# Kernel tuning notes

Hardware: AMD Instinct MI355X
Metric: run time of the kernel (lower is better)

The kernel has to match this reference:

```python
import jax, jax.numpy as jnp
import numpy as np

N_NODES = 50000
N_EDGES = 200000
IN_DIM = 16
NODE_DIM = 64
EDGE_DIM = 16
HIDDEN = 256
NUM_LAYERS = 4  # 1 NNConv + 3 GINConv


def setup_inputs() -> dict:
    key = jax.random.key(0)
    ks = jax.random.split(key, 20)
    s = 0.05
    inp = {
        "x": jax.random.normal(ks[0], (N_NODES, IN_DIM), dtype=jnp.float32),
        "edge_index": jax.random.randint(ks[1], (2, N_EDGES), 0, N_NODES, dtype=jnp.int64),
        "edge_attr": jax.random.normal(ks[2], (N_EDGES, EDGE_DIM), dtype=jnp.float32),
        # edge-NN (per-edge weight generator): attr_dim -> 256 -> 1024 -> in*out, ELU after each
        "enn_w1": jax.random.normal(ks[3], (EDGE_DIM, 256), dtype=jnp.float32) * s,
        "enn_b1": jnp.zeros((256,), dtype=jnp.float32),
        "enn_w2": jax.random.normal(ks[4], (256, 1024), dtype=jnp.float32) * s,
        "enn_b2": jnp.zeros((1024,), dtype=jnp.float32),
        "enn_w3": jax.random.normal(ks[5], (1024, IN_DIM * NODE_DIM), dtype=jnp.float32) * s,
        "enn_b3": jnp.zeros((IN_DIM * NODE_DIM,), dtype=jnp.float32),
        # NNConv root weight + bias
        "root_w": jax.random.normal(ks[6], (IN_DIM, NODE_DIM), dtype=jnp.float32) * s,
        "root_b": jnp.zeros((NODE_DIM,), dtype=jnp.float32),
        # 3 GIN MLPs (stacked): node_dim -> hidden -> hidden -> node_dim
        "gin_w1": jax.random.normal(ks[7], (3, NODE_DIM, HIDDEN), dtype=jnp.float32) * s,
        "gin_b1": jnp.zeros((3, HIDDEN), dtype=jnp.float32),
        "gin_w2": jax.random.normal(ks[8], (3, HIDDEN, HIDDEN), dtype=jnp.float32) * s,
        "gin_b2": jnp.zeros((3, HIDDEN), dtype=jnp.float32),
        "gin_w3": jax.random.normal(ks[9], (3, HIDDEN, NODE_DIM), dtype=jnp.float32) * s,
        "gin_b3": jnp.zeros((3, NODE_DIM), dtype=jnp.float32),
    }
    return inp


def _elu(x):
    return jax.nn.elu(x)


def reference(x, edge_index, edge_attr,
              enn_w1, enn_b1, enn_w2, enn_b2, enn_w3, enn_b3,
              root_w, root_b,
              gin_w1, gin_b1, gin_w2, gin_b2, gin_w3, gin_b3):
    src = edge_index[0]  # x_j (message source)
    dst = edge_index[1]  # i (aggregation target)

    # ---- Layer 0: NNConv with per-edge MLP-generated weights ----
    h = _elu(edge_attr @ enn_w1 + enn_b1)
    h = _elu(h @ enn_w2 + enn_b2)
    w_e = _elu(h @ enn_w3 + enn_b3).reshape(-1, IN_DIM, NODE_DIM)  # [E, in, out]
    msg = jnp.einsum('ei,eio->eo', x[src], w_e)                    # [E, node_dim]
    agg = jax.ops.segment_sum(msg, dst, num_segments=N_NODES)     # scatter-add
    x_cur = x @ root_w + agg + root_b                              # [N, node_dim]
    node_emb = [x_cur]

    # ---- Layers 1..3: GINConv (eps=0) with 3-layer MLP ----
    for l in range(NUM_LAYERS - 1):
        x_in = _elu(x_cur)
        nbr = jax.ops.segment_sum(x_in[src], dst, num_segments=N_NODES)
        h = x_in + nbr  # (1 + eps) * x + sum_j x_j, eps = 0
        h = _elu(h @ gin_w1[l] + gin_b1[l])
        h = _elu(h @ gin_w2[l] + gin_b2[l])
        x_cur = h @ gin_w3[l] + gin_b3[l]
        node_emb.append(x_cur)

    return jnp.stack(node_emb, axis=2)  # [N, node_dim, num_layers]
```

## Files before the change

kernel.cpp:

```cpp
#include <hip/hip_runtime.h>
#include <hip/hip_bf16.h>


#define NN 50000
#define EE 200000

typedef unsigned short u16;
typedef __attribute__((ext_vector_type(8))) short frag8;
typedef __attribute__((ext_vector_type(4))) float f32x4;

__device__ __forceinline__ float bf2f(u16 u) {
    union { unsigned int i; float f; } v; v.i = ((unsigned int)u) << 16; return v.f;
}
__device__ __forceinline__ u16 f2bf(float f) {
    union { float f; unsigned int i; } v; v.f = f;
    return (u16)((v.i + 0x7fffu + ((v.i >> 16) & 1u)) >> 16);
}
__device__ __forceinline__ float eluf(float v) {
    return v > 0.f ? v : __expf(v) - 1.f;
}

__global__ void probe_f32(const u16* __restrict__ raw, int* __restrict__ cnt) {
    int t = threadIdx.x;
    int c = 0;
    for (int j = t; j < 1024; j += 256) {
        unsigned e = (raw[j] >> 7) & 0xFF;
        if (e >= 0xBF) c++;
    }
    if (c) atomicAdd(cnt, c);
}
__global__ void cvt_bf16(const void* __restrict__ src, u16* __restrict__ dst, long n,
                         const int* __restrict__ cnt) {
    long i = (long)blockIdx.x * 256 + threadIdx.x;
    if (i >= n) return;
    if (*cnt >= 8) dst[i] = f2bf(((const float*)src)[i]);
    else           dst[i] = ((const u16*)src)[i];
}

__global__ void detect_idx64(const unsigned long long* __restrict__ p, int* __restrict__ flag) {
    long t = (long)blockIdx.x * 256 + threadIdx.x;
    if (t < EE) {
        unsigned long long v = p[t];
        if (v >> 31) atomicOr(flag, 1);
    }
}
__global__ void convert_idx(const void* __restrict__ raw, const int* __restrict__ flag,
                            int* __restrict__ s_out, int* __restrict__ d_out) {
    long t = (long)blockIdx.x * 256 + threadIdx.x;
    if (t >= EE) return;
    if (*flag) {
        const int* q = (const int*)raw;
        s_out[t] = q[t];
        d_out[t] = q[EE + t];
    } else {
        const long long* q = (const long long*)raw;
        s_out[t] = (int)q[t];
        d_out[t] = (int)q[EE + t];
    }
}

__global__ void transpose_bf16(const u16* __restrict__ in, u16* __restrict__ out, int K, int N) {
    long idx = (long)blockIdx.x * 256 + threadIdx.x;
    if (idx < (long)K * N) {
        int k = (int)(idx / N);
        int n = (int)(idx % N);
        out[(long)n * K + k] = in[idx];
    }
}

__global__ void edge_mlp1(const u16* __restrict__ attr, const u16* __restrict__ w1,
                          const u16* __restrict__ b1, u16* __restrict__ h1, int ce) {
    __shared__ u16 sa[256];
    const int t = threadIdx.x;
    const int e0 = blockIdx.x * 16;
    const int cnt = min(16, ce - e0);
    sa[t] = (t < cnt * 16) ? attr[(long)e0 * 16 + t] : (u16)0;
    float w[16];
    #pragma unroll
    for (int i = 0; i < 16; ++i) w[i] = bf2f(w1[i * 256 + t]);
    const float bb = bf2f(b1[t]);
    __syncthreads();
    for (int e = 0; e < cnt; ++e) {
        float v = bb;
        #pragma unroll
        for (int i = 0; i < 16; ++i) v += bf2f(sa[e * 16 + i]) * w[i];
        h1[(long)(e0 + e) * 256 + t] = f2bf(eluf(v));
    }
}

__device__ __forceinline__ void stage_tile(const u16* g, long row_base, long max_row,
                                           int kstride, int k0, u16* s, int t) {
    int wave = t >> 6;
    #pragma unroll
    for (int j = 0; j < 2; ++j) {
        int c = t + 256 * j;
        long r = row_base + (c >> 2);
        if (r > max_row) r = max_row;
        const u16* gp = g + r * (long)kstride + k0 + (c & 3) * 8;
        __builtin_amdgcn_global_load_lds(
            (__attribute__((address_space(1))) void*)(void*)gp,
            (__attribute__((address_space(3))) void*)((char*)s + wave * 1024 + j * 4096),
            16, 0, 0);
    }
}

__global__ __launch_bounds__(256)
void gemm_bt_bias_elu(const u16* __restrict__ A, const u16* __restrict__ BT,
                      const u16* __restrict__ bias, u16* __restrict__ C,
                      int M, int K, int N, int mpx, int lognt) {
    const int bid = blockIdx.x;
    const int xcd = bid & 7;
    const int j = bid >> 3;
    const int m_idx = xcd * mpx + (j >> lognt);
    const int n_idx = j & ((1 << lognt) - 1);
    const int num_m = (M + 127) >> 7;
    if (m_idx >= num_m) return;

    __shared__ __align__(16) u16 sA[128 * 32];
    __shared__ __align__(16) u16 sB[128 * 32];
    const int t = threadIdx.x;
    const int lane = t & 63;
    const int wave = t >> 6;
    const int wr = wave >> 1, wc = wave & 1;
    const int quad = lane >> 4, l16 = lane & 15;
    const long m0 = (long)m_idx * 128;
    const int n0 = n_idx * 128;

    f32x4 acc[4][4];
    const f32x4 z4 = {0.f, 0.f, 0.f, 0.f};
    #pragma unroll
    for (int mi = 0; mi < 4; ++mi)
        #pragma unroll
        for (int ni = 0; ni < 4; ++ni)
            acc[mi][ni] = z4;

    for (int k0 = 0; k0 < K; k0 += 32) {
        stage_tile(A, m0, (long)M - 1, K, k0, sA, t);
        stage_tile(BT, n0, (long)N - 1, K, k0, sB, t);
        __syncthreads();
        frag8 af[4], bfv[4];
        #pragma unroll
        for (int mi = 0; mi < 4; ++mi)
            af[mi] = *(const frag8*)(sA + (wr * 64 + mi * 16 + l16) * 32 + quad * 8);
        #pragma unroll
        for (int ni = 0; ni < 4; ++ni)
            bfv[ni] = *(const frag8*)(sB + (wc * 64 + ni * 16 + l16) * 32 + quad * 8);
        #pragma unroll
        for (int mi = 0; mi < 4; ++mi)
            #pragma unroll
            for (int ni = 0; ni < 4; ++ni)
                acc[mi][ni] = __builtin_amdgcn_mfma_f32_16x16x32_bf16(af[mi], bfv[ni], acc[mi][ni], 0, 0, 0);
        __syncthreads();
    }

    #pragma unroll
    for (int mi = 0; mi < 4; ++mi) {
        #pragma unroll
        for (int r = 0; r < 4; ++r) {
            long row = m0 + wr * 64 + mi * 16 + quad * 4 + r;
            if (row < M) {
                #pragma unroll
                for (int ni = 0; ni < 4; ++ni) {
                    int col = n0 + wc * 64 + ni * 16 + l16;
                    float v = acc[mi][ni][r] + bf2f(bias[col]);
                    C[row * (long)N + col] = f2bf(eluf(v));
                }
            }
        }
    }
}


#define QPHASE(PA, PB, QM, QN, LDA, LDB, VMW, STREG, SG, SRBASE, SRMAX, SKT)     \
  do {                                                                           \
    if (LDA) {                                                                   \
      _Pragma("unroll")                                                          \
      for (int mi = 0; mi < 4; ++mi) {                                           \
        _Pragma("unroll")                                                        \
        for (int kk = 0; kk < 2; ++kk) {                                         \
          int row = ((QM) * 4 + mi) * 16 + l16;                                  \
          int slot = ((kk << 2) + quad) ^ (l16 & 7);                             \
          av[mi][kk] = *(const frag8*)((const char*)(PA) + row * 128 + slot * 16); \
        }                                                                        \
      }                                                                          \
    }                                                                            \
    if ((LDB) >= 0) {                                                            \
      _Pragma("unroll")                                                          \
      for (int ni = 0; ni < 2; ++ni) {                                           \
        _Pragma("unroll")                                                        \
        for (int kk = 0; kk < 2; ++kk) {                                         \
          int row = (wn & 1) * 64 + (((LDB) & 1) * 2 + ni) * 16 + l16;           \
          int slot = ((kk << 2) + quad) ^ (l16 & 7);                             \
          bv[(LDB) & 1][ni][kk] =                                                \
              *(const frag8*)((const char*)(PB) + row * 128 + slot * 16);        \
        }                                                                        \
      }                                                                          \
    }                                                                            \
    if (VMW) asm volatile("s_waitcnt vmcnt(2)" ::: "memory");                    \
    __builtin_amdgcn_s_barrier();                                                \
    __builtin_amdgcn_s_setprio(1);                                               \
    _Pragma("unroll")                                                            \
    for (int kk = 0; kk < 2; ++kk) {                                             \
      _Pragma("unroll")                                                          \
      for (int mi = 0; mi < 4; ++mi) {                                           \
        _Pragma("unroll")                                                        \
        for (int ni = 0; ni < 2; ++ni) {                                         \
          acc[(QM) * 4 + mi][(QN) * 2 + ni] =                                    \
              __builtin_amdgcn_mfma_f32_16x16x32_bf16(                           \
                  av[mi][kk], bv[(QN)][ni][kk],                                  \
                  acc[(QM) * 4 + mi][(QN) * 2 + ni], 0, 0, 0);                   \
        }                                                                        \
      }                                                                          \
    }                                                                            \
    __builtin_amdgcn_s_setprio(0);                                               \
    stage((STREG), (SG), (SRBASE), (SRMAX), (SKT));                              \
  } while (0)

__global__ __launch_bounds__(512, 2)
void gemm256p(const u16* __restrict__ A, const u16* __restrict__ BT,
              const u16* __restrict__ bias, u16* __restrict__ C,
              int M, int K, int N, int mpx, int lognt) {
    const int bid = blockIdx.x;
    const int xcd = bid & 7;
    const int j = bid >> 3;
    const int m_idx = xcd * mpx + (j >> lognt);
    const int n_idx = j & ((1 << lognt) - 1);
    const int num_m = (M + 255) >> 8;
    if (m_idx >= num_m) return;

    __shared__ __align__(16) u16 lds[2][4][8192];
    const int t = threadIdx.x;
    const int lane = t & 63;
    const int wave = t >> 6;
    const int wm = wave >> 2;
    const int wn = wave & 3;
    const int quad = lane >> 4, l16 = lane & 15;
    const long m0 = (long)m_idx * 256;
    const long n0 = (long)n_idx * 256;

    const int gslot = (((lane & 7) ^ ((lane >> 3) & 7)) << 3);

    auto stage = [&](u16* reg, const u16* G, long rbase, long rmax, int kt) {
        #pragma unroll
        for (int jj = 0; jj < 2; ++jj) {
            const int ck = wave * 2 + jj;
            long r = rbase + ck * 8 + (lane >> 3);
            if (r > rmax) r = rmax;
            const u16* gp = G + r * (long)K + ((long)kt << 6) + gslot;
            __builtin_amdgcn_global_load_lds(
                (__attribute__((address_space(1))) void*)(void*)gp,
                (__attribute__((address_space(3))) void*)((char*)reg + ck * 1024),
                16, 0, 0);
        }
    };

    f32x4 acc[8][4];
    const f32x4 z4 = {0.f, 0.f, 0.f, 0.f};
    #pragma unroll
    for (int mi = 0; mi < 8; ++mi)
        #pragma unroll
        for (int ni = 0; ni < 4; ++ni)
            acc[mi][ni] = z4;
    frag8 av[4][2];
    frag8 bv[2][2][2];

    const int ntk = K >> 6;
    const int niter = ntk >> 1;
    const long MM = (long)M - 1, NMX = (long)N - 1;

    stage(&lds[0][2][0], BT, n0,       NMX, 0);
    stage(&lds[0][3][0], BT, n0 + 128, NMX, 0);
    stage(&lds[0][0][0], A,  m0,       MM,  0);
    stage(&lds[0][1][0], A,  m0 + 128, MM,  0);
    stage(&lds[1][2][0], BT, n0,       NMX, 1);
    stage(&lds[1][3][0], BT, n0 + 128, NMX, 1);
    asm volatile("s_waitcnt vmcnt(4)" ::: "memory");
    __builtin_amdgcn_s_barrier();

    const u16* paX = &lds[0][wm][0];
    const u16* pbX = &lds[0][2 + (wn >> 1)][0];
    const u16* paY = &lds[1][wm][0];
    const u16* pbY = &lds[1][2 + (wn >> 1)][0];

    for (int it = 0; it < niter; ++it) {
        const int t1k = 2 * it + 1;
        int t2k = 2 * it + 2; if (t2k > ntk - 1) t2k = ntk - 1;
        int t3k = 2 * it + 3; if (t3k > ntk - 1) t3k = ntk - 1;

        QPHASE(paX, pbX, 0, 0, 1,  0, 0, &lds[1][0][0], A,  m0,       MM,  t1k);
        QPHASE(paX, pbX, 0, 1, 0,  1, 0, &lds[1][1][0], A,  m0 + 128, MM,  t1k);
        QPHASE(paX, pbX, 1, 0, 1, -1, 0, &lds[0][2][0], BT, n0,       NMX, t2k);
        QPHASE(paX, pbX, 1, 1, 0, -1, 1, &lds[0][3][0], BT, n0 + 128, NMX, t2k);
        QPHASE(paY, pbY, 0, 0, 1,  0, 0, &lds[0][0][0], A,  m0,       MM,  t2k);
        QPHASE(paY, pbY, 0, 1, 0,  1, 0, &lds[0][1][0], A,  m0 + 128, MM,  t2k);
        QPHASE(paY, pbY, 1, 0, 1, -1, 0, &lds[1][2][0], BT, n0,       NMX, t3k);
        QPHASE(paY, pbY, 1, 1, 0, -1, 1, &lds[1][3][0], BT, n0 + 128, NMX, t3k);
    }
    asm volatile("s_waitcnt vmcnt(0)" ::: "memory");

    #pragma unroll
    for (int mi = 0; mi < 8; ++mi) {
        #pragma unroll
        for (int r = 0; r < 4; ++r) {
            long row = m0 + wm * 128 + mi * 16 + quad * 4 + r;
            if (row < M) {
                #pragma unroll
                for (int ni = 0; ni < 4; ++ni) {
                    long col = n0 + wn * 64 + ni * 16 + l16;
                    float v = acc[mi][ni][r] + bf2f(bias[col]);
                    C[row * (long)N + col] = f2bf(eluf(v));
                }
            }
        }
    }
}

__global__ __launch_bounds__(256)
void gemm_bt_f32(const u16* __restrict__ A, const u16* __restrict__ BT,
                 const u16* __restrict__ bias, float* __restrict__ C,
                 int M, int K) {
    __shared__ __align__(16) u16 sA[256 * 32];
    __shared__ __align__(16) u16 sB[64 * 32];
    const int t = threadIdx.x;
    const int lane = t & 63;
    const int wave = t >> 6;
    const int quad = lane >> 4, l16 = lane & 15;
    const long m0 = (long)blockIdx.x * 256;

    f32x4 acc[4][4];
    const f32x4 z4 = {0.f, 0.f, 0.f, 0.f};
    #pragma unroll
    for (int mi = 0; mi < 4; ++mi)
        #pragma unroll
        for (int ni = 0; ni < 4; ++ni)
            acc[mi][ni] = z4;

    for (int k0 = 0; k0 < K; k0 += 32) {
        #pragma unroll
        for (int j = 0; j < 4; ++j) {
            int c = t + 256 * j;
            long r = m0 + (c >> 2);
            if (r > (long)M - 1) r = (long)M - 1;
            const u16* gp = A + r * (long)K + k0 + (c & 3) * 8;
            __builtin_amdgcn_global_load_lds(
                (__attribute__((address_space(1))) void*)(void*)gp,
                (__attribute__((address_space(3))) void*)((char*)sA + wave * 1024 + j * 4096),
                16, 0, 0);
        }
        {
            int c = t;
            const u16* gp = BT + (long)(c >> 2) * K + k0 + (c & 3) * 8;
            __builtin_amdgcn_global_load_lds(
                (__attribute__((address_space(1))) void*)(void*)gp,
                (__attribute__((address_space(3))) void*)((char*)sB + wave * 1024),
                16, 0, 0);
        }
        __syncthreads();
        frag8 af[4], bfv[4];
        #pragma unroll
        for (int mi = 0; mi < 4; ++mi)
            af[mi] = *(const frag8*)(sA + (wave * 64 + mi * 16 + l16) * 32 + quad * 8);
        #pragma unroll
        for (int ni = 0; ni < 4; ++ni)
            bfv[ni] = *(const frag8*)(sB + (ni * 16 + l16) * 32 + quad * 8);
        #pragma unroll
        for (int mi = 0; mi < 4; ++mi)
            #pragma unroll
            for (int ni = 0; ni < 4; ++ni)
                acc[mi][ni] = __builtin_amdgcn_mfma_f32_16x16x32_bf16(af[mi], bfv[ni], acc[mi][ni], 0, 0, 0);
        __syncthreads();
    }

    #pragma unroll
    for (int mi = 0; mi < 4; ++mi) {
        #pragma unroll
        for (int r = 0; r < 4; ++r) {
            long row = m0 + wave * 64 + mi * 16 + quad * 4 + r;
            if (row < M) {
                #pragma unroll
                for (int ni = 0; ni < 4; ++ni) {
                    int col = ni * 16 + l16;
                    C[row * 64 + col] = acc[mi][ni][r] + bf2f(bias[col]);
                }
            }
        }
    }
}

__global__ void nnconv_msg(const u16* __restrict__ we, const u16* __restrict__ x,
                           const int* __restrict__ src, const int* __restrict__ dst,
                           float* __restrict__ agg, int ce) {
    long idx = (long)blockIdx.x * 256 + threadIdx.x;
    if (idx >= (long)ce * 64) return;
    int o = (int)(idx & 63);
    long e = idx >> 6;
    const u16* wr = we + e * 1024;
    const u16* xr = x + (long)src[e] * 16;
    float v = 0.f;
    #pragma unroll
    for (int i = 0; i < 16; ++i)
        v += bf2f(xr[i]) * bf2f(wr[i * 64 + o]);
    atomicAdd(&agg[(long)dst[e] * 64 + o], v);
}

__global__ void add_root(const u16* __restrict__ x, const u16* __restrict__ rw,
                         const u16* __restrict__ rb, float* __restrict__ xcur) {
    long idx = (long)blockIdx.x * 256 + threadIdx.x;
    if (idx >= (long)NN * 64) return;
    int d = (int)(idx & 63);
    long n = idx >> 6;
    float v = bf2f(rb[d]);
    #pragma unroll
    for (int i = 0; i < 16; ++i)
        v += bf2f(x[n * 16 + i]) * bf2f(rw[i * 64 + d]);
    xcur[idx] += v;
}

__global__ void elu_bf16(const float* __restrict__ in, u16* __restrict__ o, long n) {
    long idx = (long)blockIdx.x * 256 + threadIdx.x;
    if (idx < n) o[idx] = f2bf(eluf(in[idx]));
}

__global__ void gin_scatter(const u16* __restrict__ xin, const int* __restrict__ src,
                            const int* __restrict__ dst, float* __restrict__ nbr) {
    long idx = (long)blockIdx.x * 256 + threadIdx.x;
    if (idx >= (long)EE * 64) return;
    int d = (int)(idx & 63);
    long e = idx >> 6;
    atomicAdd(&nbr[(long)dst[e] * 64 + d], bf2f(xin[(long)src[e] * 64 + d]));
}

__global__ void gin_combine(const u16* __restrict__ xin, const float* __restrict__ nbr,
                            u16* __restrict__ hin, long n) {
    long idx = (long)blockIdx.x * 256 + threadIdx.x;
    if (idx < n) hin[idx] = f2bf(bf2f(xin[idx]) + nbr[idx]);
}

__global__ void write_out(const float* __restrict__ e0, const float* __restrict__ e1,
                          const float* __restrict__ e2, const float* __restrict__ e3,
                          float* __restrict__ out) {
    long idx = (long)blockIdx.x * 256 + threadIdx.x;
    if (idx >= (long)NN * 64) return;
    float4 v = {e0[idx], e1[idx], e2[idx], e3[idx]};
    *(float4*)(out + idx * 4) = v;
}

extern "C" void kernel_launch(void* const* d_in, const int* in_sizes, int n_in,
                              void* d_out, int out_size, void* d_ws, size_t ws_size,
                              hipStream_t stream) {
    (void)in_sizes; (void)n_in; (void)out_size;
    const void* eidx = d_in[1];
    float* out = (float*)d_out;

    char* ws = (char*)d_ws;
    size_t off = 0;
    auto alloc = [&](size_t bytes) {
        char* p = ws + off;
        off += (bytes + 255) & ~(size_t)255;
        return p;
    };
    int* src32 = (int*)alloc((size_t)EE * 4);
    int* dst32 = (int*)alloc((size_t)EE * 4);
    int* flag  = (int*)alloc(256);
    int* cnt   = (int*)alloc(256);
    const int cv_idx[16] = {0, 2, 3, 4, 5, 6, 7, 8, 9, 10, 11, 12, 13, 14, 15, 16};
    const long cv_n[16]  = {800000, 3200000, 4096, 256, 262144, 1024, 1048576, 1024,
                            1024, 64, 49152, 768, 196608, 768, 49152, 192};
    u16* cv[16];
    for (int i = 0; i < 16; ++i) cv[i] = (u16*)alloc((size_t)cv_n[i] * 2);
    u16 *xc = cv[0], *eac = cv[1], *w1c = cv[2], *b1c = cv[3], *w2c = cv[4], *b2c = cv[5],
        *w3c = cv[6], *b3c = cv[7], *rwc = cv[8], *rbc = cv[9],
        *g1c = cv[10], *gb1c = cv[11], *g2c = cv[12], *gb2c = cv[13], *g3c = cv[14], *gb3c = cv[15];
    u16* w2t = (u16*)alloc((size_t)1024 * 256 * 2);
    u16* w3t = (u16*)alloc((size_t)1024 * 1024 * 2);
    u16* g1t = (u16*)alloc((size_t)3 * 256 * 64 * 2);
    u16* g2t = (u16*)alloc((size_t)3 * 256 * 256 * 2);
    u16* g3t = (u16*)alloc((size_t)3 * 64 * 256 * 2);
    float* emb[4];
    for (int l = 0; l < 4; ++l) emb[l] = (float*)alloc((size_t)NN * 64 * 4);
    float* agg = emb[0];
    char* scratch = (char*)alloc(0);
    size_t avail = (ws_size > off + 4096) ? (ws_size - off - 4096) : 0;

    long CE = (long)(avail / 4608) & ~127L;
    if (CE < 128) CE = 128;
    if (CE > 200064) CE = 200064;
    u16* h1c = (u16*)scratch;
    u16* h2c = (u16*)(scratch + (size_t)CE * 512);
    u16* wec = (u16*)(scratch + (size_t)CE * 2560);

    long gin_fixed = (long)NN * 64 * 4 + (long)NN * 64 * 2;
    long gin_avail = (long)avail - gin_fixed;
    if (gin_avail < 0) gin_avail = 0;
    long CN = (gin_avail / 1152) & ~255L;
    if (CN < 256) CN = 256;
    if (CN > 50176) CN = 50176;
    float* nbr = (float*)scratch;
    u16* xin   = (u16*)(scratch + (size_t)NN * 64 * 4);
    u16* hin   = (u16*)(scratch + gin_fixed);
    u16* hg1   = hin + (size_t)CN * 64;
    u16* hg2   = hg1 + (size_t)CN * 256;

    auto cdiv = [](long a, long b) { return (unsigned)((a + b - 1) / b); };

    hipMemsetAsync(cnt, 0, 4, stream);
    probe_f32<<<1, 256, 0, stream>>>((const u16*)d_in[0], cnt);
    for (int i = 0; i < 16; ++i)
        cvt_bf16<<<cdiv(cv_n[i], 256), 256, 0, stream>>>(d_in[cv_idx[i]], cv[i], cv_n[i], cnt);

    hipMemsetAsync(flag, 0, 4, stream);
    detect_idx64<<<cdiv(EE, 256), 256, 0, stream>>>((const unsigned long long*)eidx, flag);
    convert_idx<<<cdiv(EE, 256), 256, 0, stream>>>(eidx, flag, src32, dst32);

    transpose_bf16<<<cdiv(256 * 1024, 256), 256, 0, stream>>>(w2c, w2t, 256, 1024);
    transpose_bf16<<<cdiv(1024 * 1024, 256), 256, 0, stream>>>(w3c, w3t, 1024, 1024);
    for (int l = 0; l < 3; ++l) {
        transpose_bf16<<<cdiv(64 * 256, 256), 256, 0, stream>>>(g1c + l * 64 * 256, g1t + l * 256 * 64, 64, 256);
        transpose_bf16<<<cdiv(256 * 256, 256), 256, 0, stream>>>(g2c + l * 256 * 256, g2t + l * 256 * 256, 256, 256);
        transpose_bf16<<<cdiv(256 * 64, 256), 256, 0, stream>>>(g3c + l * 256 * 64, g3t + l * 64 * 256, 256, 64);
    }

    hipMemsetAsync(agg, 0, (size_t)NN * 64 * 4, stream);
    for (long e0 = 0; e0 < EE; e0 += CE) {
        int ce = (int)((EE - e0 < CE) ? (EE - e0) : CE);
        int mpx2 = cdiv(cdiv(ce, 256), 8);
        edge_mlp1<<<cdiv(ce, 16), 256, 0, stream>>>(eac + e0 * 16, w1c, b1c, h1c, ce);
        gemm256p<<<8 * mpx2 * 4, 512, 0, stream>>>(h1c, w2t, b2c, h2c, ce, 256, 1024, mpx2, 2);
        gemm256p<<<8 * mpx2 * 4, 512, 0, stream>>>(h2c, w3t, b3c, wec, ce, 1024, 1024, mpx2, 2);
        nnconv_msg<<<cdiv((long)ce * 64, 256), 256, 0, stream>>>(wec, xc, src32 + e0, dst32 + e0, agg, ce);
    }
    add_root<<<cdiv((long)NN * 64, 256), 256, 0, stream>>>(xc, rwc, rbc, agg);

    for (int l = 0; l < 3; ++l) {
        elu_bf16<<<cdiv((long)NN * 64, 256), 256, 0, stream>>>(emb[l], xin, (long)NN * 64);
        hipMemsetAsync(nbr, 0, (size_t)NN * 64 * 4, stream);
        gin_scatter<<<cdiv((long)EE * 64, 256), 256, 0, stream>>>(xin, src32, dst32, nbr);
        for (long n0 = 0; n0 < NN; n0 += CN) {
            int cn = (int)((NN - n0 < CN) ? (NN - n0) : CN);
            int mpx = cdiv(cdiv(cn, 128), 8);
            gin_combine<<<cdiv((long)cn * 64, 256), 256, 0, stream>>>(xin + n0 * 64, nbr + n0 * 64, hin, (long)cn * 64);
            gemm_bt_bias_elu<<<8 * mpx * 2, 256, 0, stream>>>(hin, g1t + l * 256 * 64, gb1c + l * 256, hg1, cn, 64, 256, mpx, 1);
            gemm_bt_bias_elu<<<8 * mpx * 2, 256, 0, stream>>>(hg1, g2t + l * 256 * 256, gb2c + l * 256, hg2, cn, 256, 256, mpx, 1);
            gemm_bt_f32<<<cdiv(cn, 256), 256, 0, stream>>>(hg2, g3t + l * 64 * 256, gb3c + l * 64, emb[l + 1] + n0 * 64, cn, 256);
        }
    }
    write_out<<<cdiv((long)NN * 64, 256), 256, 0, stream>>>(emb[0], emb[1], emb[2], emb[3], out);
}
```

Before: 1.509 ms.

## Restructure gemm256p pipeline, precompute LDS offsets, use it for GIN hidden GEMM

The 256x256 tiled GEMM now precomputes per-lane swizzled LDS fragment addresses instead of recomputing row and slot arithmetic each phase. Each phase issues its global-to-LDS stage before the MFMA block, with a deeper vmcnt wait and an extra barrier after compute. Row clamping is skipped for tiles that lie fully in bounds. The GIN second-layer GEMM (256x256) switches from the smaller gemm_bt_bias_elu to gemm256p. The goals are earlier prefetch issue and fewer address ops, at the cost of an extra barrier per phase and a launch with fewer, larger blocks for the GIN GEMM.

```diff
diff --git a/kernel.cpp b/kernel.cpp
--- a/kernel.cpp
+++ b/kernel.cpp
@@ -171,32 +171,24 @@
 }
 
 
-#define QPHASE(PA, PB, QM, QN, LDA, LDB, VMW, STREG, SG, SRBASE, SRMAX, SKT)     \
+#define QPHASE(PA0, PA1, PB0, PB1, QM, QN, LDA, LDB, VMW, STREG, SG, SRB, SRM, SCL, SKT) \
   do {                                                                           \
     if (LDA) {                                                                   \
       _Pragma("unroll")                                                          \
       for (int mi = 0; mi < 4; ++mi) {                                           \
-        _Pragma("unroll")                                                        \
-        for (int kk = 0; kk < 2; ++kk) {                                         \
-          int row = ((QM) * 4 + mi) * 16 + l16;                                  \
-          int slot = ((kk << 2) + quad) ^ (l16 & 7);                             \
-          av[mi][kk] = *(const frag8*)((const char*)(PA) + row * 128 + slot * 16); \
-        }                                                                        \
+        av[mi][0] = *(const frag8*)((PA0) + ((QM) * 4 + mi) * 2048);             \
+        av[mi][1] = *(const frag8*)((PA1) + ((QM) * 4 + mi) * 2048);             \
       }                                                                          \
     }                                                                            \
     if ((LDB) >= 0) {                                                            \
       _Pragma("unroll")                                                          \
       for (int ni = 0; ni < 2; ++ni) {                                           \
-        _Pragma("unroll")                                                        \
-        for (int kk = 0; kk < 2; ++kk) {                                         \
-          int row = (wn & 1) * 64 + (((LDB) & 1) * 2 + ni) * 16 + l16;           \
-          int slot = ((kk << 2) + quad) ^ (l16 & 7);                             \
-          bv[(LDB) & 1][ni][kk] =                                                \
-              *(const frag8*)((const char*)(PB) + row * 128 + slot * 16);        \
-        }                                                                        \
+        bv[(LDB) & 1][ni][0] = *(const frag8*)((PB0) + (((LDB) & 1) * 2 + ni) * 2048); \
+        bv[(LDB) & 1][ni][1] = *(const frag8*)((PB1) + (((LDB) & 1) * 2 + ni) * 2048); \
       }                                                                          \
     }                                                                            \
-    if (VMW) asm volatile("s_waitcnt vmcnt(2)" ::: "memory");                    \
+    stage((STREG), (SG), (SRB), (SRM), (SKT), (SCL));                            \
+    if (VMW) asm volatile("s_waitcnt vmcnt(4)" ::: "memory");                    \
     __builtin_amdgcn_s_barrier();                                                \
     __builtin_amdgcn_s_setprio(1);                                               \
     _Pragma("unroll")                                                            \
@@ -213,7 +205,7 @@
       }                                                                          \
     }                                                                            \
     __builtin_amdgcn_s_setprio(0);                                               \
-    stage((STREG), (SG), (SRBASE), (SRMAX), (SKT));                              \
+    __builtin_amdgcn_s_barrier();                                                \
   } while (0)
 
 __global__ __launch_bounds__(512, 2)
@@ -238,18 +230,37 @@
     const long m0 = (long)m_idx * 256;
     const long n0 = (long)n_idx * 256;
 
+    const int aoff0 = l16 * 128 + ((quad ^ (l16 & 3)) << 4) + (((l16 >> 2) & 1) << 6);
+    const int aoff1 = aoff0 ^ 64;
+    const int bex = (wn & 1) * 8192;
+    const char* pAX0 = (const char*)&lds[0][wm][0] + aoff0;
+    const char* pAX1 = (const char*)&lds[0][wm][0] + aoff1;
+    const char* pAY0 = (const char*)&lds[1][wm][0] + aoff0;
+    const char* pAY1 = (const char*)&lds[1][wm][0] + aoff1;
+    const char* pBX0 = (const char*)&lds[0][2 + (wn >> 1)][0] + aoff0 + bex;
+    const char* pBX1 = (const char*)&lds[0][2 + (wn >> 1)][0] + aoff1 + bex;
+    const char* pBY0 = (const char*)&lds[1][2 + (wn >> 1)][0] + aoff0 + bex;
+    const char* pBY1 = (const char*)&lds[1][2 + (wn >> 1)][0] + aoff1 + bex;
+
     const int gslot = (((lane & 7) ^ ((lane >> 3) & 7)) << 3);
-
-    auto stage = [&](u16* reg, const u16* G, long rbase, long rmax, int kt) {
+    const int lane_row = lane >> 3;
+    const long lane_go = (long)lane_row * K + gslot;
+
+    auto stage = [&](u16* sreg, const u16* G, long rbase, long rmax, int kt, bool cl) {
         #pragma unroll
         for (int jj = 0; jj < 2; ++jj) {
             const int ck = wave * 2 + jj;
-            long r = rbase + ck * 8 + (lane >> 3);
-            if (r > rmax) r = rmax;
-            const u16* gp = G + r * (long)K + ((long)kt << 6) + gslot;
+            const u16* gp;
+            if (!cl) {
+                gp = G + (rbase + ck * 8) * (long)K + ((long)kt << 6) + lane_go;
+            } else {
+                long r = rbase + ck * 8 + lane_row;
+                if (r > rmax) r = rmax;
+                gp = G + r * (long)K + ((long)kt << 6) + gslot;
+            }
             __builtin_amdgcn_global_load_lds(
                 (__attribute__((address_space(1))) void*)(void*)gp,
-                (__attribute__((address_space(3))) void*)((char*)reg + ck * 1024),
+                (__attribute__((address_space(3))) void*)((char*)sreg + ck * 1024),
                 16, 0, 0);
         }
     };
@@ -267,34 +278,30 @@
     const int ntk = K >> 6;
     const int niter = ntk >> 1;
     const long MM = (long)M - 1, NMX = (long)N - 1;
-
-    stage(&lds[0][2][0], BT, n0,       NMX, 0);
-    stage(&lds[0][3][0], BT, n0 + 128, NMX, 0);
-    stage(&lds[0][0][0], A,  m0,       MM,  0);
-    stage(&lds[0][1][0], A,  m0 + 128, MM,  0);
-    stage(&lds[1][2][0], BT, n0,       NMX, 1);
-    stage(&lds[1][3][0], BT, n0 + 128, NMX, 1);
+    const bool aclamp = (m0 + 255) > MM;
+
+    stage(&lds[0][2][0], BT, n0,       NMX, 0, false);
+    stage(&lds[0][3][0], BT, n0 + 128, NMX, 0, false);
+    stage(&lds[0][0][0], A,  m0,       MM,  0, aclamp);
+    stage(&lds[0][1][0], A,  m0 + 128, MM,  0, aclamp);
+    stage(&lds[1][2][0], BT, n0,       NMX, 1, false);
+    stage(&lds[1][3][0], BT, n0 + 128, NMX, 1, false);
     asm volatile("s_waitcnt vmcnt(4)" ::: "memory");
     __builtin_amdgcn_s_barrier();
-
-    const u16* paX = &lds[0][wm][0];
-    const u16* pbX = &lds[0][2 + (wn >> 1)][0];
-    const u16* paY = &lds[1][wm][0];
-    const u16* pbY = &lds[1][2 + (wn >> 1)][0];
 
     for (int it = 0; it < niter; ++it) {
         const int t1k = 2 * it + 1;
         int t2k = 2 * it + 2; if (t2k > ntk - 1) t2k = ntk - 1;
         int t3k = 2 * it + 3; if (t3k > ntk - 1) t3k = ntk - 1;
 
-        QPHASE(paX, pbX, 0, 0, 1,  0, 0, &lds[1][0][0], A,  m0,       MM,  t1k);
-        QPHASE(paX, pbX, 0, 1, 0,  1, 0, &lds[1][1][0], A,  m0 + 128, MM,  t1k);
-        QPHASE(paX, pbX, 1, 0, 1, -1, 0, &lds[0][2][0], BT, n0,       NMX, t2k);
-        QPHASE(paX, pbX, 1, 1, 0, -1, 1, &lds[0][3][0], BT, n0 + 128, NMX, t2k);
-        QPHASE(paY, pbY, 0, 0, 1,  0, 0, &lds[0][0][0], A,  m0,       MM,  t2k);
-        QPHASE(paY, pbY, 0, 1, 0,  1, 0, &lds[0][1][0], A,  m0 + 128, MM,  t2k);
-        QPHASE(paY, pbY, 1, 0, 1, -1, 0, &lds[1][2][0], BT, n0,       NMX, t3k);
-        QPHASE(paY, pbY, 1, 1, 0, -1, 1, &lds[1][3][0], BT, n0 + 128, NMX, t3k);
+        QPHASE(pAX0, pAX1, pBX0, pBX1, 0, 0, 1,  0, 0, &lds[1][0][0], A,  m0,       MM,  aclamp, t1k);
+        QPHASE(pAX0, pAX1, pBX0, pBX1, 0, 1, 0,  1, 0, &lds[1][1][0], A,  m0 + 128, MM,  aclamp, t1k);
+        QPHASE(pAX0, pAX1, pBX0, pBX1, 1, 0, 1, -1, 0, &lds[0][2][0], BT, n0,       NMX, false,  t2k);
+        QPHASE(pAX0, pAX1, pBX0, pBX1, 1, 1, 0, -1, 1, &lds[0][3][0], BT, n0 + 128, NMX, false,  t2k);
+        QPHASE(pAY0, pAY1, pBY0, pBY1, 0, 0, 1,  0, 0, &lds[0][0][0], A,  m0,       MM,  aclamp, t2k);
+        QPHASE(pAY0, pAY1, pBY0, pBY1, 0, 1, 0,  1, 0, &lds[0][1][0], A,  m0 + 128, MM,  aclamp, t2k);
+        QPHASE(pAY0, pAY1, pBY0, pBY1, 1, 0, 1, -1, 0, &lds[1][2][0], BT, n0,       NMX, false,  t3k);
+        QPHASE(pAY0, pAY1, pBY0, pBY1, 1, 1, 0, -1, 1, &lds[1][3][0], BT, n0 + 128, NMX, false,  t3k);
     }
     asm volatile("s_waitcnt vmcnt(0)" ::: "memory");
 
@@ -538,9 +545,10 @@
         for (long n0 = 0; n0 < NN; n0 += CN) {
             int cn = (int)((NN - n0 < CN) ? (NN - n0) : CN);
             int mpx = cdiv(cdiv(cn, 128), 8);
+            int mpx2 = cdiv(cdiv(cn, 256), 8);
             gin_combine<<<cdiv((long)cn * 64, 256), 256, 0, stream>>>(xin + n0 * 64, nbr + n0 * 64, hin, (long)cn * 64);
             gemm_bt_bias_elu<<<8 * mpx * 2, 256, 0, stream>>>(hin, g1t + l * 256 * 64, gb1c + l * 256, hg1, cn, 64, 256, mpx, 1);
-            gemm_bt_bias_elu<<<8 * mpx * 2, 256, 0, stream>>>(hg1, g2t + l * 256 * 256, gb2c + l * 256, hg2, cn, 256, 256, mpx, 1);
+            gemm256p<<<8 * mpx2 * 1, 512, 0, stream>>>(hg1, g2t + l * 256 * 256, gb2c + l * 256, hg2, cn, 256, 256, mpx2, 0);
             gemm_bt_f32<<<cdiv(cn, 256), 256, 0, stream>>>(hg2, g3t + l * 64 * 256, gb3c + l * 64, emb[l + 1] + n0 * 64, cn, 256);
         }
     }
```

Result: no change. 1.538 ms (+1.9%).
